# Kernel tuning notes

Measured on AMD Instinct MI355X. Metric: run time of the kernel, lower is better.

The kernel has to match this reference:

```python
import jax, jax.numpy as jnp
import numpy as np

B, S, D_IN, D_OUT = 4, 2048, 4096, 4096


def setup_inputs() -> dict:
    key = jax.random.key(0)
    k1, k2, k3, k4 = jax.random.split(key, 4)
    x = jax.random.normal(k1, (B, S, D_IN), dtype=jnp.float32) * 0.02
    base = jax.random.normal(k2, (D_IN, D_OUT), dtype=jnp.float32) * 0.02
    # mask holds the sign bits of the weight delta: 1 -> +1, 0 -> -1
    mask = jax.random.randint(k3, (D_IN, D_OUT), 0, 2, dtype=jnp.int32)
    # coeff = mean(|diff|); a small positive scalar
    coeff = jnp.abs(jax.random.normal(k4, (), dtype=jnp.float32)) * 0.01
    return {"x": x, "base": base, "coeff": coeff, "mask": mask}


def reference(x, base, coeff, mask):
    # binary_bmm(x, packed_mask) == x @ sign, sign = 2*mask - 1 in {-1, +1}
    sign = (2 * mask - 1).astype(x.dtype)            # [D_IN, D_OUT]
    return x @ base + coeff * (x @ sign)             # [B, S, D_OUT]
```

## Files before the change

### kernel.cpp

```cpp
#include <hip/hip_runtime.h>
#include <hip/hip_bf16.h>
#include <stdint.h>

#define M_DIM 8192
#define K_DIM 4096
#define N_DIM 4096
#define NT (K_DIM / 64)

typedef __attribute__((ext_vector_type(8))) short short8;
typedef __attribute__((ext_vector_type(4))) float f32x4;
typedef unsigned short ushort_t;

typedef const __attribute__((address_space(1))) unsigned int as1const_u32;
typedef __attribute__((address_space(3))) unsigned int as3_u32;

__device__ __forceinline__ unsigned short f2bf(float f) {
  unsigned int u = __float_as_uint(f);
  u += 0x7FFF + ((u >> 16) & 1);
  return (unsigned short)(u >> 16);
}

__global__ void cvt_x_kernel(const float* __restrict__ x,
                             ushort_t* __restrict__ xb, long n8) {
  long i = (long)blockIdx.x * blockDim.x + threadIdx.x;
  long stride = (long)gridDim.x * blockDim.x;
  for (; i < n8; i += stride) {
    const float4* p = (const float4*)(x + i * 8);
    float4 v0 = p[0], v1 = p[1];
    short8 o;
    o[0] = (short)f2bf(v0.x); o[1] = (short)f2bf(v0.y);
    o[2] = (short)f2bf(v0.z); o[3] = (short)f2bf(v0.w);
    o[4] = (short)f2bf(v1.x); o[5] = (short)f2bf(v1.y);
    o[6] = (short)f2bf(v1.z); o[7] = (short)f2bf(v1.w);
    *(short8*)(xb + i * 8) = o;
  }
}

__global__ void make_wt_kernel(const float* __restrict__ base,
                               const int* __restrict__ mask,
                               const float* __restrict__ coeffp,
                               ushort_t* __restrict__ wt) {
  __shared__ ushort_t tile[32][33];
  const float c = *coeffp;
  const int n0 = blockIdx.x * 32, k0 = blockIdx.y * 32;
  const int tx = threadIdx.x, ty = threadIdx.y;
#pragma unroll
  for (int r = 0; r < 4; ++r) {
    int k = k0 + ty + r * 8;
    int n = n0 + tx;
    size_t idx = (size_t)k * N_DIM + n;
    float s = mask[idx] ? c : -c;
    tile[ty + r * 8][tx] = f2bf(base[idx] + s);
  }
  __syncthreads();
#pragma unroll
  for (int r = 0; r < 4; ++r) {
    int n = n0 + ty + r * 8;
    int k = k0 + tx;
    wt[(size_t)n * K_DIM + k] = tile[tx][ty + r * 8];
  }
}

#define FENCE asm volatile("" ::: "memory")
#define BAR   do { FENCE; __builtin_amdgcn_s_barrier(); FENCE; } while (0)
#define VW6   asm volatile("s_waitcnt vmcnt(6)" ::: "memory")
#define VW0   asm volatile("s_waitcnt vmcnt(0)" ::: "memory")

__global__ __launch_bounds__(512, 2) void gemm_bf16_256(
    const ushort_t* __restrict__ Xb,
    const ushort_t* __restrict__ Wt,
    float* __restrict__ out) {
  __shared__ ushort_t Al[2][256][64];
  __shared__ ushort_t Bl[2][256][64];

  const int tid = threadIdx.x;
  const int lane = tid & 63;
  const int w = tid >> 6;
  const int wm = w >> 2, wn = w & 3;
  const int lrow = lane & 15, kg = lane >> 4;

  const int bid = blockIdx.x;
  const int swz = (bid & 7) * 64 + (bid >> 3);
  const int bm = (swz >> 4) * 256;
  const int bn = (swz & 15) * 256;

  const int rh0 = w * 8 + (lane >> 3);
  const int srcslot = (lane & 7) ^ ((lane >> 3) & 7);
  const ushort_t* Ag = Xb + (size_t)(bm + rh0) * K_DIM + srcslot * 8;
  const ushort_t* Bg = Wt + (size_t)(bn + rh0) * K_DIM + srcslot * 8;
  char* AlB = (char*)&Al[0][0][0];
  char* BlB = (char*)&Bl[0][0][0];
  const int ldsw = w * 1024;

#define STAGE(Og, Lb, u, h) do {                                                   \
    const ushort_t* _s0 = (Og) + (size_t)((h) * 128) * K_DIM + (size_t)(u) * 64;   \
    __builtin_amdgcn_global_load_lds((as1const_u32*)_s0,                           \
        (as3_u32*)((Lb) + ((u) & 1) * 32768 + (h) * 16384 + ldsw), 16, 0, 0);      \
    __builtin_amdgcn_global_load_lds((as1const_u32*)(_s0 + (size_t)64 * K_DIM),    \
        (as3_u32*)((Lb) + ((u) & 1) * 32768 + (h) * 16384 + ldsw + 8192), 16, 0, 0); \
  } while (0)

  const int arow = (wm * 16 + lrow) << 7;
  const int brow = (wn * 16 + lrow) << 7;
  const int sw0 = ((0 + kg) ^ (lrow & 7)) << 4;
  const int sw1 = ((4 + kg) ^ (lrow & 7)) << 4;

#define LDA(bt, mi, kk) (*(const short8*)(AlB + (bt) * 32768 + (mi) * 4096 + arow + ((kk) ? sw1 : sw0)))
#define LDB(bt, ni, kk) (*(const short8*)(BlB + (bt) * 32768 + (ni) * 8192 + brow + ((kk) ? sw1 : sw0)))
#define MFMA(a, b, c) __builtin_amdgcn_mfma_f32_16x16x32_bf16(a, b, c, 0, 0, 0)

  f32x4 acc[8][4] = {};
  short8 Ar[4][2], Br[4][2];

  STAGE(Ag, AlB, 0, 0); STAGE(Bg, BlB, 0, 0);
  STAGE(Bg, BlB, 0, 1); STAGE(Ag, AlB, 0, 1);
  STAGE(Ag, AlB, 1, 0); STAGE(Bg, BlB, 1, 0);
  STAGE(Bg, BlB, 1, 1);
  VW6; BAR;

  for (int t = 0; t < NT - 2; ++t) {
    const int bt = t & 1;

#pragma unroll
    for (int mi = 0; mi < 4; ++mi) { Ar[mi][0] = LDA(bt, mi, 0); Ar[mi][1] = LDA(bt, mi, 1); }
#pragma unroll
    for (int ni = 0; ni < 2; ++ni) { Br[ni][0] = LDB(bt, ni, 0); Br[ni][1] = LDB(bt, ni, 1); }
    STAGE(Ag, AlB, t + 1, 1);
    BAR;
    __builtin_amdgcn_s_setprio(1);
#pragma unroll
    for (int mi = 0; mi < 4; ++mi)
#pragma unroll
      for (int ni = 0; ni < 2; ++ni) {
        acc[mi][ni] = MFMA(Ar[mi][0], Br[ni][0], acc[mi][ni]);
        acc[mi][ni] = MFMA(Ar[mi][1], Br[ni][1], acc[mi][ni]);
      }
    __builtin_amdgcn_s_setprio(0);
    BAR;

#pragma unroll
    for (int ni = 2; ni < 4; ++ni) { Br[ni][0] = LDB(bt, ni, 0); Br[ni][1] = LDB(bt, ni, 1); }
    STAGE(Ag, AlB, t + 2, 0);
    STAGE(Bg, BlB, t + 2, 0);
    BAR;
    __builtin_amdgcn_s_setprio(1);
#pragma unroll
    for (int mi = 0; mi < 4; ++mi)
#pragma unroll
      for (int ni = 2; ni < 4; ++ni) {
        acc[mi][ni] = MFMA(Ar[mi][0], Br[ni][0], acc[mi][ni]);
        acc[mi][ni] = MFMA(Ar[mi][1], Br[ni][1], acc[mi][ni]);
      }
    __builtin_amdgcn_s_setprio(0);
    BAR;

#pragma unroll
    for (int mi = 0; mi < 4; ++mi) { Ar[mi][0] = LDA(bt, mi + 4, 0); Ar[mi][1] = LDA(bt, mi + 4, 1); }
    STAGE(Bg, BlB, t + 2, 1);
    BAR;
    __builtin_amdgcn_s_setprio(1);
#pragma unroll
    for (int mi = 0; mi < 4; ++mi)
#pragma unroll
      for (int ni = 0; ni < 4; ++ni) {
        acc[mi + 4][ni] = MFMA(Ar[mi][0], Br[ni][0], acc[mi + 4][ni]);
        acc[mi + 4][ni] = MFMA(Ar[mi][1], Br[ni][1], acc[mi + 4][ni]);
      }
    __builtin_amdgcn_s_setprio(0);
    VW6; BAR;
  }

  STAGE(Ag, AlB, NT - 1, 1);
  VW0; BAR;
  for (int tt = NT - 2; tt < NT; ++tt) {
    const int bt = tt & 1;
#pragma unroll
    for (int mi = 0; mi < 4; ++mi) { Ar[mi][0] = LDA(bt, mi, 0); Ar[mi][1] = LDA(bt, mi, 1); }
#pragma unroll
    for (int ni = 0; ni < 4; ++ni) { Br[ni][0] = LDB(bt, ni, 0); Br[ni][1] = LDB(bt, ni, 1); }
#pragma unroll
    for (int mi = 0; mi < 4; ++mi)
#pragma unroll
      for (int ni = 0; ni < 4; ++ni) {
        acc[mi][ni] = MFMA(Ar[mi][0], Br[ni][0], acc[mi][ni]);
        acc[mi][ni] = MFMA(Ar[mi][1], Br[ni][1], acc[mi][ni]);
      }
#pragma unroll
    for (int mi = 0; mi < 4; ++mi) { Ar[mi][0] = LDA(bt, mi + 4, 0); Ar[mi][1] = LDA(bt, mi + 4, 1); }
#pragma unroll
    for (int mi = 0; mi < 4; ++mi)
#pragma unroll
      for (int ni = 0; ni < 4; ++ni) {
        acc[mi + 4][ni] = MFMA(Ar[mi][0], Br[ni][0], acc[mi + 4][ni]);
        acc[mi + 4][ni] = MFMA(Ar[mi][1], Br[ni][1], acc[mi + 4][ni]);
      }
  }

#pragma unroll
  for (int mi = 0; mi < 8; ++mi)
#pragma unroll
    for (int ni = 0; ni < 4; ++ni) {
      const int gr = bm + mi * 32 + wm * 16 + kg * 4;
      const int gc = bn + ni * 64 + wn * 16 + lrow;
      float* o = out + (size_t)gr * N_DIM + gc;
#pragma unroll
      for (int r = 0; r < 4; ++r) o[(size_t)r * N_DIM] = acc[mi][ni][r];
    }
}

__global__ void gemm_f32_fallback(const float* __restrict__ x,
                                  const float* __restrict__ base,
                                  const float* __restrict__ coeffp,
                                  const int* __restrict__ mask,
                                  float* __restrict__ out) {
  __shared__ float As[32][33];
  __shared__ float Bs[32][33];
  const float c = *coeffp;
  const int tx = threadIdx.x, ty = threadIdx.y;
  const int row = blockIdx.y * 32 + ty, col = blockIdx.x * 32 + tx;
  float acc = 0.f;
  for (int kt = 0; kt < K_DIM; kt += 32) {
    As[ty][tx] = x[(size_t)row * K_DIM + kt + tx];
    size_t bidx = (size_t)(kt + ty) * N_DIM + col;
    Bs[ty][tx] = base[bidx] + (mask[bidx] ? c : -c);
    __syncthreads();
#pragma unroll
    for (int k = 0; k < 32; ++k) acc += As[ty][k] * Bs[k][tx];
    __syncthreads();
  }
  out[(size_t)row * N_DIM + col] = acc;
}

extern "C" void kernel_launch(void* const* d_in, const int* in_sizes, int n_in,
                              void* d_out, int out_size, void* d_ws, size_t ws_size,
                              hipStream_t stream) {
  const float* x     = (const float*)d_in[0];
  const float* base  = (const float*)d_in[1];
  const float* coeff = (const float*)d_in[2];
  const int*   mask  = (const int*)d_in[3];
  float* out = (float*)d_out;

  const size_t xb_bytes = (size_t)M_DIM * K_DIM * sizeof(ushort_t);
  const size_t wt_bytes = (size_t)K_DIM * N_DIM * sizeof(ushort_t);

  if (ws_size >= xb_bytes + wt_bytes) {
    ushort_t* xb = (ushort_t*)d_ws;
    ushort_t* wt = (ushort_t*)((char*)d_ws + xb_bytes);
    long n8 = (long)M_DIM * K_DIM / 8;
    cvt_x_kernel<<<4096, 256, 0, stream>>>(x, xb, n8);
    make_wt_kernel<<<dim3(N_DIM / 32, K_DIM / 32), dim3(32, 8), 0, stream>>>(base, mask, coeff, wt);
    gemm_bf16_256<<<512, 512, 0, stream>>>(xb, wt, out);
  } else {
    gemm_f32_fallback<<<dim3(N_DIM / 32, M_DIM / 32), dim3(32, 32), 0, stream>>>(x, base, coeff, mask, out);
  }
}
```

Baseline: 303.7 us.

## Restructure GEMM main loop into four quadrant phases with double-buffered fragment registers

The main loop is split into four MFMA quadrants with two sets of A and B register fragments. The next tile's first A and B fragments are read from LDS during the previous iteration, so LDS reads overlap MFMA work. Global-to-LDS staging is reordered across the phases and the prologue and epilogue are adjusted to match. The change raises register pressure and makes the correctness of the waitcnt and barrier sequence more delicate.

```diff
diff --git a/kernel.cpp b/kernel.cpp
--- a/kernel.cpp
+++ b/kernel.cpp
@@ -64,6 +64,7 @@
 #define FENCE asm volatile("" ::: "memory")
 #define BAR   do { FENCE; __builtin_amdgcn_s_barrier(); FENCE; } while (0)
 #define VW6   asm volatile("s_waitcnt vmcnt(6)" ::: "memory")
+#define VW4   asm volatile("s_waitcnt vmcnt(4)" ::: "memory")
 #define VW0   asm volatile("s_waitcnt vmcnt(0)" ::: "memory")
 
 __global__ __launch_bounds__(512, 2) void gemm_bf16_256(
@@ -109,91 +110,92 @@
 #define LDB(bt, ni, kk) (*(const short8*)(BlB + (bt) * 32768 + (ni) * 8192 + brow + ((kk) ? sw1 : sw0)))
 #define MFMA(a, b, c) __builtin_amdgcn_mfma_f32_16x16x32_bf16(a, b, c, 0, 0, 0)
 
+  short8 Ar0[4][2], Ar1[4][2];
+  short8 Br0[2][2], Br1[2][2];
   f32x4 acc[8][4] = {};
-  short8 Ar[4][2], Br[4][2];
+
+#define RD_A(dst, bt, base)                                                        \
+  _Pragma("unroll")                                                                \
+  for (int mi = 0; mi < 4; ++mi) {                                                 \
+    dst[mi][0] = LDA(bt, (base) + mi, 0); dst[mi][1] = LDA(bt, (base) + mi, 1);    \
+  }
+#define RD_B(dst, bt, base)                                                        \
+  _Pragma("unroll")                                                                \
+  for (int ni = 0; ni < 2; ++ni) {                                                 \
+    dst[ni][0] = LDB(bt, (base) + ni, 0); dst[ni][1] = LDB(bt, (base) + ni, 1);    \
+  }
+#define MMQ(mb, nb, Aset, Bset)                                                    \
+  _Pragma("unroll")                                                                \
+  for (int mi = 0; mi < 4; ++mi)                                                   \
+    _Pragma("unroll")                                                              \
+    for (int ni = 0; ni < 2; ++ni) {                                               \
+      acc[(mb) + mi][(nb) + ni] = MFMA(Aset[mi][0], Bset[ni][0], acc[(mb) + mi][(nb) + ni]); \
+      acc[(mb) + mi][(nb) + ni] = MFMA(Aset[mi][1], Bset[ni][1], acc[(mb) + mi][(nb) + ni]); \
+    }
 
   STAGE(Ag, AlB, 0, 0); STAGE(Bg, BlB, 0, 0);
   STAGE(Bg, BlB, 0, 1); STAGE(Ag, AlB, 0, 1);
   STAGE(Ag, AlB, 1, 0); STAGE(Bg, BlB, 1, 0);
-  STAGE(Bg, BlB, 1, 1);
-  VW6; BAR;
+  VW4; BAR;
+  RD_A(Ar0, 0, 0);
+  RD_B(Br0, 0, 0);
 
   for (int t = 0; t < NT - 2; ++t) {
-    const int bt = t & 1;
-
-#pragma unroll
-    for (int mi = 0; mi < 4; ++mi) { Ar[mi][0] = LDA(bt, mi, 0); Ar[mi][1] = LDA(bt, mi, 1); }
-#pragma unroll
-    for (int ni = 0; ni < 2; ++ni) { Br[ni][0] = LDB(bt, ni, 0); Br[ni][1] = LDB(bt, ni, 1); }
+    const int bt = t & 1, bo = bt ^ 1;
+
+    RD_B(Br1, bt, 2);
+    STAGE(Bg, BlB, t + 1, 1);
+    BAR;
+    __builtin_amdgcn_s_setprio(1);
+    MMQ(0, 0, Ar0, Br0);
+    __builtin_amdgcn_s_setprio(0);
+    VW6; BAR;
+
+    RD_A(Ar1, bt, 4);
     STAGE(Ag, AlB, t + 1, 1);
     BAR;
     __builtin_amdgcn_s_setprio(1);
-#pragma unroll
-    for (int mi = 0; mi < 4; ++mi)
-#pragma unroll
-      for (int ni = 0; ni < 2; ++ni) {
-        acc[mi][ni] = MFMA(Ar[mi][0], Br[ni][0], acc[mi][ni]);
-        acc[mi][ni] = MFMA(Ar[mi][1], Br[ni][1], acc[mi][ni]);
-      }
-    __builtin_amdgcn_s_setprio(0);
-    BAR;
-
-#pragma unroll
-    for (int ni = 2; ni < 4; ++ni) { Br[ni][0] = LDB(bt, ni, 0); Br[ni][1] = LDB(bt, ni, 1); }
+    MMQ(0, 2, Ar0, Br1);
+    __builtin_amdgcn_s_setprio(0);
+    VW6; BAR;
+
     STAGE(Ag, AlB, t + 2, 0);
+    BAR;
+    __builtin_amdgcn_s_setprio(1);
+    MMQ(4, 0, Ar1, Br0);
+    __builtin_amdgcn_s_setprio(0);
+    RD_A(Ar0, bo, 0);
+    BAR;
+
     STAGE(Bg, BlB, t + 2, 0);
     BAR;
     __builtin_amdgcn_s_setprio(1);
-#pragma unroll
-    for (int mi = 0; mi < 4; ++mi)
-#pragma unroll
-      for (int ni = 2; ni < 4; ++ni) {
-        acc[mi][ni] = MFMA(Ar[mi][0], Br[ni][0], acc[mi][ni]);
-        acc[mi][ni] = MFMA(Ar[mi][1], Br[ni][1], acc[mi][ni]);
-      }
-    __builtin_amdgcn_s_setprio(0);
-    BAR;
-
-#pragma unroll
-    for (int mi = 0; mi < 4; ++mi) { Ar[mi][0] = LDA(bt, mi + 4, 0); Ar[mi][1] = LDA(bt, mi + 4, 1); }
-    STAGE(Bg, BlB, t + 2, 1);
-    BAR;
-    __builtin_amdgcn_s_setprio(1);
-#pragma unroll
-    for (int mi = 0; mi < 4; ++mi)
-#pragma unroll
-      for (int ni = 0; ni < 4; ++ni) {
-        acc[mi + 4][ni] = MFMA(Ar[mi][0], Br[ni][0], acc[mi + 4][ni]);
-        acc[mi + 4][ni] = MFMA(Ar[mi][1], Br[ni][1], acc[mi + 4][ni]);
-      }
-    __builtin_amdgcn_s_setprio(0);
-    VW6; BAR;
-  }
-
+    MMQ(4, 2, Ar1, Br1);
+    __builtin_amdgcn_s_setprio(0);
+    VW6;
+    RD_B(Br0, bo, 0);
+    BAR;
+  }
+
+  STAGE(Bg, BlB, NT - 1, 1);
   STAGE(Ag, AlB, NT - 1, 1);
   VW0; BAR;
-  for (int tt = NT - 2; tt < NT; ++tt) {
-    const int bt = tt & 1;
-#pragma unroll
-    for (int mi = 0; mi < 4; ++mi) { Ar[mi][0] = LDA(bt, mi, 0); Ar[mi][1] = LDA(bt, mi, 1); }
-#pragma unroll
-    for (int ni = 0; ni < 4; ++ni) { Br[ni][0] = LDB(bt, ni, 0); Br[ni][1] = LDB(bt, ni, 1); }
-#pragma unroll
-    for (int mi = 0; mi < 4; ++mi)
-#pragma unroll
-      for (int ni = 0; ni < 4; ++ni) {
-        acc[mi][ni] = MFMA(Ar[mi][0], Br[ni][0], acc[mi][ni]);
-        acc[mi][ni] = MFMA(Ar[mi][1], Br[ni][1], acc[mi][ni]);
-      }
-#pragma unroll
-    for (int mi = 0; mi < 4; ++mi) { Ar[mi][0] = LDA(bt, mi + 4, 0); Ar[mi][1] = LDA(bt, mi + 4, 1); }
-#pragma unroll
-    for (int mi = 0; mi < 4; ++mi)
-#pragma unroll
-      for (int ni = 0; ni < 4; ++ni) {
-        acc[mi + 4][ni] = MFMA(Ar[mi][0], Br[ni][0], acc[mi + 4][ni]);
-        acc[mi + 4][ni] = MFMA(Ar[mi][1], Br[ni][1], acc[mi + 4][ni]);
-      }
+  {
+    const int bt = (NT - 2) & 1, bl = (NT - 1) & 1;
+    RD_B(Br1, bt, 2);
+    RD_A(Ar1, bt, 4);
+    MMQ(0, 0, Ar0, Br0);
+    MMQ(0, 2, Ar0, Br1);
+    MMQ(4, 0, Ar1, Br0);
+    MMQ(4, 2, Ar1, Br1);
+    RD_A(Ar0, bl, 0);
+    RD_B(Br0, bl, 0);
+    RD_B(Br1, bl, 2);
+    RD_A(Ar1, bl, 4);
+    MMQ(0, 0, Ar0, Br0);
+    MMQ(0, 2, Ar0, Br1);
+    MMQ(4, 0, Ar1, Br0);
+    MMQ(4, 2, Ar1, Br1);
   }
 
 #pragma unroll
```

Measured after the change: 341.4 us. +12.4%, slower.
